# Optimization experiments

Measured on AMD Instinct MI355X. Metric: run time of the kernel, lower is better.

Reference implementation:

```python
import jax, jax.numpy as jnp
import numpy as np

V, E, H, L = 80, 8, 256, 2
B, S = 2048, 256


def setup_inputs() -> dict:
    key = jax.random.key(0)
    ks = jax.random.split(key, 8)
    x = jax.random.randint(ks[0], (B, S), 0, V, dtype=jnp.int32)
    emb = jax.random.normal(ks[1], (V, E), jnp.float32) * 0.1

    def cell_params(k, din):
        k1, k2 = jax.random.split(k)
        W_ih = jax.random.normal(k1, (4 * H, din), jnp.float32) * (1.0 / np.sqrt(din))
        W_hh = jax.random.normal(k2, (4 * H, H), jnp.float32) * (1.0 / np.sqrt(H))
        # biases zero except forget gate (second quarter) set to 1, as in _initialize_weights
        b_ih = jnp.zeros((4 * H,), jnp.float32).at[H:2 * H].set(1.0)
        b_hh = jnp.zeros((4 * H,), jnp.float32).at[H:2 * H].set(1.0)
        return W_ih, W_hh, b_ih, b_hh

    W_ih0, W_hh0, b_ih0, b_hh0 = cell_params(ks[2], E)
    W_ih1, W_hh1, b_ih1, b_hh1 = cell_params(ks[3], H)
    fc_w = jax.random.normal(ks[4], (V, H), jnp.float32) * (1.0 / np.sqrt(H))
    fc_b = jnp.zeros((V,), jnp.float32)
    return dict(x=x, emb=emb,
                W_ih0=W_ih0, W_hh0=W_hh0, b_ih0=b_ih0, b_hh0=b_hh0,
                W_ih1=W_ih1, W_hh1=W_hh1, b_ih1=b_ih1, b_hh1=b_hh1,
                fc_w=fc_w, fc_b=fc_b)


def _lstm_cell(x_t, h, c, W_ih, W_hh, b_ih, b_hh):
    # PyTorch LSTMCell gate order: i, f, g, o
    gates = x_t @ W_ih.T + b_ih + h @ W_hh.T + b_hh  # [B, 4H]
    i_g, f_g, g_g, o_g = jnp.split(gates, 4, axis=-1)
    c_new = jax.nn.sigmoid(f_g) * c + jax.nn.sigmoid(i_g) * jnp.tanh(g_g)
    h_new = jax.nn.sigmoid(o_g) * jnp.tanh(c_new)
    return h_new, c_new


def reference(x, emb, W_ih0, W_hh0, b_ih0, b_hh0, W_ih1, W_hh1, b_ih1, b_hh1, fc_w, fc_b):
    batch = x.shape[0]
    layers = ((W_ih0, W_hh0, b_ih0, b_hh0), (W_ih1, W_hh1, b_ih1, b_hh1))
    e = emb[x]                       # [B, S, E]
    e_t = jnp.swapaxes(e, 0, 1)      # [S, B, E] time-major for scan

    h0 = tuple(jnp.zeros((batch, H), e.dtype) for _ in range(L))
    c0 = tuple(jnp.zeros((batch, H), e.dtype) for _ in range(L))

    def step(carry, x_t):
        hs, cs = carry
        inp = x_t
        new_h, new_c = [], []
        for i, (Wi, Wh, bi, bh) in enumerate(layers):
            h_i, c_i = _lstm_cell(inp, hs[i], cs[i], Wi, Wh, bi, bh)
            new_h.append(h_i)
            new_c.append(c_i)
            inp = h_i
        return (tuple(new_h), tuple(new_c)), None

    (h_fin, c_fin), _ = jax.lax.scan(step, (h0, c0), e_t)
    # dropout is identity in eval mode; fc on last layer's final hidden state
    logits = h_fin[-1] @ fc_w.T + fc_b    # [B, V]
    return logits, (jnp.stack(h_fin), jnp.stack(c_fin))
```

## Files before the change

### kernel.cpp

```cpp
#include <hip/hip_runtime.h>
#include <math.h>

#define VCAB 80
#define EDIM 8
#define HDIM 256
#define BAT 2048
#define SEQ 256
#define BT 8
#define NWG (BAT/BT)
#define NTHR 512

#define W0T_K 264
#define W1T_K 512
#define W0T_OFF 0
#define W1T_OFF (W0T_K*1024)
#define BIAS0_OFF (W1T_OFF + W1T_K*1024)
#define BIAS1_OFF (BIAS0_OFF + 1024)
#define WS_FLOATS (BIAS1_OFF + 1024)

__global__ void prep_kernel(const float* __restrict__ Wih0, const float* __restrict__ Whh0,
                            const float* __restrict__ bih0, const float* __restrict__ bhh0,
                            const float* __restrict__ Wih1, const float* __restrict__ Whh1,
                            const float* __restrict__ bih1, const float* __restrict__ bhh1,
                            float* __restrict__ ws) {
  int idx = blockIdx.x * 256 + threadIdx.x;
  if (idx < W0T_K * 1024) {
    int k = idx >> 10, n2 = idx & 1023;
    int unit = n2 >> 2, g = n2 & 3, r = g * HDIM + unit;
    float v = (k < EDIM) ? Wih0[r * EDIM + k] : Whh0[r * HDIM + (k - EDIM)];
    ws[W0T_OFF + idx] = v;
  } else if (idx < W0T_K * 1024 + W1T_K * 1024) {
    int i2 = idx - W0T_K * 1024;
    int k = i2 >> 10, n2 = i2 & 1023;
    int unit = n2 >> 2, g = n2 & 3, r = g * HDIM + unit;
    float v = (k < HDIM) ? Wih1[r * HDIM + k] : Whh1[r * HDIM + (k - HDIM)];
    ws[W1T_OFF + i2] = v;
  } else if (idx < W0T_K * 1024 + W1T_K * 1024 + 1024) {
    int n2 = idx - (W0T_K * 1024 + W1T_K * 1024);
    int unit = n2 >> 2, g = n2 & 3, r = g * HDIM + unit;
    ws[BIAS0_OFF + n2] = bih0[r] + bhh0[r];
  } else if (idx < W0T_K * 1024 + W1T_K * 1024 + 2048) {
    int n2 = idx - (W0T_K * 1024 + W1T_K * 1024 + 1024);
    int unit = n2 >> 2, g = n2 & 3, r = g * HDIM + unit;
    ws[BIAS1_OFF + n2] = bih1[r] + bhh1[r];
  }
}

__device__ __forceinline__ float sigm(float x) {
  return 1.0f / (1.0f + __expf(-x));
}
__device__ __forceinline__ float tanh_f(float x) {
  float ax = fabsf(x);
  float e = __expf(-2.0f * ax);
  float t = 1.0f - 2.0f * e / (1.0f + e);
  return copysignf(t, x);
}

#define FMA4(A, HS, W) \
  A.x += (HS) * (W).x; A.y += (HS) * (W).y; A.z += (HS) * (W).z; A.w += (HS) * (W).w;

__global__ __launch_bounds__(NTHR, 2) void lstm_kernel(
    const int* __restrict__ x, const float* __restrict__ emb,
    const float* __restrict__ ws,
    const float* __restrict__ fcw, const float* __restrict__ fcb,
    float* __restrict__ out) {
  __shared__ float inp0[BT][W0T_K];
  __shared__ float inp1[BT][W1T_K];
  __shared__ float4 red[BT][HDIM];

  const int tid = threadIdx.x;
  const int grp = tid >> 8;
  const int utid = tid & 255;
  const int bg = blockIdx.x * BT;
  const float4* __restrict__ W0 = (const float4*)(ws + W0T_OFF);
  const float4* __restrict__ W1 = (const float4*)(ws + W1T_OFF);

  float c0[BT], c1[BT];
#pragma unroll
  for (int b = 0; b < BT; b++) { c0[b] = 0.f; c1[b] = 0.f; }
  if (grp == 0) {
#pragma unroll
    for (int b = 0; b < BT; b++) {
      inp0[b][EDIM + utid] = 0.f;
      inp1[b][utid] = 0.f;
      inp1[b][HDIM + utid] = 0.f;
    }
  }
  const float4 bias0 = ((const float4*)(ws + BIAS0_OFF))[utid];
  const float4 bias1 = ((const float4*)(ws + BIAS1_OFF))[utid];
  __syncthreads();

  for (int t = 0; t < SEQ; t++) {
    if (tid < BT * EDIM) {
      int b = tid >> 3, d = tid & 7;
      int xv = x[(bg + b) * SEQ + t];
      inp0[b][d] = emb[xv * EDIM + d];
    }
    __syncthreads();

    float4 acc[BT];
#pragma unroll
    for (int b = 0; b < BT; b++)
      acc[b] = (grp == 0) ? bias0 : make_float4(0.f, 0.f, 0.f, 0.f);
    {
      const int kbase = grp * (W0T_K / 2);
#pragma unroll 3
      for (int i = 0; i < W0T_K / 8; i++) {
        const int k = kbase + 4 * i;
        float4 wa = W0[(k + 0) * 256 + utid];
        float4 wb = W0[(k + 1) * 256 + utid];
        float4 wc = W0[(k + 2) * 256 + utid];
        float4 wd = W0[(k + 3) * 256 + utid];
#pragma unroll
        for (int b = 0; b < BT; b++) {
          float4 hv = *(const float4*)&inp0[b][k];
          FMA4(acc[b], hv.x, wa); FMA4(acc[b], hv.y, wb);
          FMA4(acc[b], hv.z, wc); FMA4(acc[b], hv.w, wd);
        }
      }
    }
    if (grp == 1) {
#pragma unroll
      for (int b = 0; b < BT; b++) red[b][utid] = acc[b];
    }
    __syncthreads();
    if (grp == 0) {
#pragma unroll
      for (int b = 0; b < BT; b++) {
        float4 p = red[b][utid];
        float ig = sigm(acc[b].x + p.x), fg = sigm(acc[b].y + p.y);
        float gg = tanh_f(acc[b].z + p.z), og = sigm(acc[b].w + p.w);
        c0[b] = fg * c0[b] + ig * gg;
        float h = og * tanh_f(c0[b]);
        inp0[b][EDIM + utid] = h;
        inp1[b][utid] = h;
      }
    }
    __syncthreads();

#pragma unroll
    for (int b = 0; b < BT; b++)
      acc[b] = (grp == 0) ? bias1 : make_float4(0.f, 0.f, 0.f, 0.f);
    {
      const int kbase = grp * (W1T_K / 2);
#pragma unroll 4
      for (int i = 0; i < W1T_K / 8; i++) {
        const int k = kbase + 4 * i;
        float4 wa = W1[(k + 0) * 256 + utid];
        float4 wb = W1[(k + 1) * 256 + utid];
        float4 wc = W1[(k + 2) * 256 + utid];
        float4 wd = W1[(k + 3) * 256 + utid];
#pragma unroll
        for (int b = 0; b < BT; b++) {
          float4 hv = *(const float4*)&inp1[b][k];
          FMA4(acc[b], hv.x, wa); FMA4(acc[b], hv.y, wb);
          FMA4(acc[b], hv.z, wc); FMA4(acc[b], hv.w, wd);
        }
      }
    }
    if (grp == 1) {
#pragma unroll
      for (int b = 0; b < BT; b++) red[b][utid] = acc[b];
    }
    __syncthreads();
    if (grp == 0) {
#pragma unroll
      for (int b = 0; b < BT; b++) {
        float4 p = red[b][utid];
        float ig = sigm(acc[b].x + p.x), fg = sigm(acc[b].y + p.y);
        float gg = tanh_f(acc[b].z + p.z), og = sigm(acc[b].w + p.w);
        c1[b] = fg * c1[b] + ig * gg;
        inp1[b][HDIM + utid] = og * tanh_f(c1[b]);
      }
    }
    __syncthreads();
  }

  for (int o = tid; o < BT * VCAB; o += NTHR) {
    int b = o / VCAB, v = o - b * VCAB;
    float a = fcb[v];
    const float4* wrow = (const float4*)(fcw + v * HDIM);
    const float4* hrow = (const float4*)&inp1[b][HDIM];
#pragma unroll 4
    for (int k = 0; k < HDIM / 4; k++) {
      float4 w = wrow[k];
      float4 h = hrow[k];
      a += h.x * w.x + h.y * w.y + h.z * w.z + h.w * w.w;
    }
    out[(bg + b) * VCAB + v] = a;
  }

  if (grp == 0) {
    float* outh = out + BAT * VCAB;
    float* outc = outh + 2 * BAT * HDIM;
#pragma unroll
    for (int b = 0; b < BT; b++) {
      outh[0 * BAT * HDIM + (bg + b) * HDIM + utid] = inp0[b][EDIM + utid];
      outh[1 * BAT * HDIM + (bg + b) * HDIM + utid] = inp1[b][HDIM + utid];
      outc[0 * BAT * HDIM + (bg + b) * HDIM + utid] = c0[b];
      outc[1 * BAT * HDIM + (bg + b) * HDIM + utid] = c1[b];
    }
  }
}

extern "C" void kernel_launch(void* const* d_in, const int* in_sizes, int n_in,
                              void* d_out, int out_size, void* d_ws, size_t ws_size,
                              hipStream_t stream) {
  const int*   x    = (const int*)d_in[0];
  const float* emb  = (const float*)d_in[1];
  const float* Wih0 = (const float*)d_in[2];
  const float* Whh0 = (const float*)d_in[3];
  const float* bih0 = (const float*)d_in[4];
  const float* bhh0 = (const float*)d_in[5];
  const float* Wih1 = (const float*)d_in[6];
  const float* Whh1 = (const float*)d_in[7];
  const float* bih1 = (const float*)d_in[8];
  const float* bhh1 = (const float*)d_in[9];
  const float* fcw  = (const float*)d_in[10];
  const float* fcb  = (const float*)d_in[11];
  float* out = (float*)d_out;
  float* ws  = (float*)d_ws;

  prep_kernel<<<(WS_FLOATS + 255) / 256, 256, 0, stream>>>(
      Wih0, Whh0, bih0, bhh0, Wih1, Whh1, bih1, bhh1, ws);
  lstm_kernel<<<NWG, NTHR, 0, stream>>>(x, emb, ws, fcw, fcb, out);
}
```

Baseline: 14.71 ms.

## Double block size and split batch rows across two thread halves

Block size goes from 512 to 1024 threads. The 8 batch rows of a workgroup are now split into two halves of 4 rows, each handled by its own 512-thread group that keeps the existing two-way K split. Each thread holds fewer accumulators and cell states, which frees registers and exposes more parallelism per step. In exchange, every weight element is loaded twice per block, once per row half, so per-step global/L2 weight traffic doubles and fewer FMAs are amortised per load.

```diff
diff --git a/kernel.cpp b/kernel.cpp
--- a/kernel.cpp
+++ b/kernel.cpp
@@ -8,7 +8,7 @@
 #define SEQ 256
 #define BT 8
 #define NWG (BAT/BT)
-#define NTHR 512
+#define NTHR 1024
 
 #define W0T_K 264
 #define W1T_K 512
@@ -59,7 +59,7 @@
 #define FMA4(A, HS, W) \
   A.x += (HS) * (W).x; A.y += (HS) * (W).y; A.z += (HS) * (W).z; A.w += (HS) * (W).w;
 
-__global__ __launch_bounds__(NTHR, 2) void lstm_kernel(
+__global__ __launch_bounds__(NTHR, 4) void lstm_kernel(
     const int* __restrict__ x, const float* __restrict__ emb,
     const float* __restrict__ ws,
     const float* __restrict__ fcw, const float* __restrict__ fcb,
@@ -69,21 +69,23 @@
   __shared__ float4 red[BT][HDIM];
 
   const int tid = threadIdx.x;
-  const int grp = tid >> 8;
   const int utid = tid & 255;
+  const int kgrp = (tid >> 8) & 1;
+  const int rh = tid >> 9;
+  const int rbase = rh * 4;
   const int bg = blockIdx.x * BT;
   const float4* __restrict__ W0 = (const float4*)(ws + W0T_OFF);
   const float4* __restrict__ W1 = (const float4*)(ws + W1T_OFF);
 
-  float c0[BT], c1[BT];
-#pragma unroll
-  for (int b = 0; b < BT; b++) { c0[b] = 0.f; c1[b] = 0.f; }
-  if (grp == 0) {
-#pragma unroll
-    for (int b = 0; b < BT; b++) {
-      inp0[b][EDIM + utid] = 0.f;
-      inp1[b][utid] = 0.f;
-      inp1[b][HDIM + utid] = 0.f;
+  float c0[4], c1[4];
+#pragma unroll
+  for (int j = 0; j < 4; j++) { c0[j] = 0.f; c1[j] = 0.f; }
+  if (kgrp == 0) {
+#pragma unroll
+    for (int j = 0; j < 4; j++) {
+      inp0[rbase + j][EDIM + utid] = 0.f;
+      inp1[rbase + j][utid] = 0.f;
+      inp1[rbase + j][HDIM + utid] = 0.f;
     }
   }
   const float4 bias0 = ((const float4*)(ws + BIAS0_OFF))[utid];
@@ -98,12 +100,12 @@
     }
     __syncthreads();
 
-    float4 acc[BT];
-#pragma unroll
-    for (int b = 0; b < BT; b++)
-      acc[b] = (grp == 0) ? bias0 : make_float4(0.f, 0.f, 0.f, 0.f);
+    float4 acc[4];
+#pragma unroll
+    for (int j = 0; j < 4; j++)
+      acc[j] = (kgrp == 0) ? bias0 : make_float4(0.f, 0.f, 0.f, 0.f);
     {
-      const int kbase = grp * (W0T_K / 2);
+      const int kbase = kgrp * (W0T_K / 2);
 #pragma unroll 3
       for (int i = 0; i < W0T_K / 8; i++) {
         const int k = kbase + 4 * i;
@@ -112,37 +114,37 @@
         float4 wc = W0[(k + 2) * 256 + utid];
         float4 wd = W0[(k + 3) * 256 + utid];
 #pragma unroll
-        for (int b = 0; b < BT; b++) {
-          float4 hv = *(const float4*)&inp0[b][k];
-          FMA4(acc[b], hv.x, wa); FMA4(acc[b], hv.y, wb);
-          FMA4(acc[b], hv.z, wc); FMA4(acc[b], hv.w, wd);
+        for (int j = 0; j < 4; j++) {
+          float4 hv = *(const float4*)&inp0[rbase + j][k];
+          FMA4(acc[j], hv.x, wa); FMA4(acc[j], hv.y, wb);
+          FMA4(acc[j], hv.z, wc); FMA4(acc[j], hv.w, wd);
         }
       }
     }
-    if (grp == 1) {
-#pragma unroll
-      for (int b = 0; b < BT; b++) red[b][utid] = acc[b];
-    }
-    __syncthreads();
-    if (grp == 0) {
-#pragma unroll
-      for (int b = 0; b < BT; b++) {
-        float4 p = red[b][utid];
-        float ig = sigm(acc[b].x + p.x), fg = sigm(acc[b].y + p.y);
-        float gg = tanh_f(acc[b].z + p.z), og = sigm(acc[b].w + p.w);
-        c0[b] = fg * c0[b] + ig * gg;
-        float h = og * tanh_f(c0[b]);
-        inp0[b][EDIM + utid] = h;
-        inp1[b][utid] = h;
-      }
-    }
-    __syncthreads();
-
-#pragma unroll
-    for (int b = 0; b < BT; b++)
-      acc[b] = (grp == 0) ? bias1 : make_float4(0.f, 0.f, 0.f, 0.f);
+    if (kgrp == 1) {
+#pragma unroll
+      for (int j = 0; j < 4; j++) red[rbase + j][utid] = acc[j];
+    }
+    __syncthreads();
+    if (kgrp == 0) {
+#pragma unroll
+      for (int j = 0; j < 4; j++) {
+        float4 p = red[rbase + j][utid];
+        float ig = sigm(acc[j].x + p.x), fg = sigm(acc[j].y + p.y);
+        float gg = tanh_f(acc[j].z + p.z), og = sigm(acc[j].w + p.w);
+        c0[j] = fg * c0[j] + ig * gg;
+        float h = og * tanh_f(c0[j]);
+        inp0[rbase + j][EDIM + utid] = h;
+        inp1[rbase + j][utid] = h;
+      }
+    }
+    __syncthreads();
+
+#pragma unroll
+    for (int j = 0; j < 4; j++)
+      acc[j] = (kgrp == 0) ? bias1 : make_float4(0.f, 0.f, 0.f, 0.f);
     {
-      const int kbase = grp * (W1T_K / 2);
+      const int kbase = kgrp * (W1T_K / 2);
 #pragma unroll 4
       for (int i = 0; i < W1T_K / 8; i++) {
         const int k = kbase + 4 * i;
@@ -151,26 +153,26 @@
         float4 wc = W1[(k + 2) * 256 + utid];
         float4 wd = W1[(k + 3) * 256 + utid];
 #pragma unroll
-        for (int b = 0; b < BT; b++) {
-          float4 hv = *(const float4*)&inp1[b][k];
-          FMA4(acc[b], hv.x, wa); FMA4(acc[b], hv.y, wb);
-          FMA4(acc[b], hv.z, wc); FMA4(acc[b], hv.w, wd);
+        for (int j = 0; j < 4; j++) {
+          float4 hv = *(const float4*)&inp1[rbase + j][k];
+          FMA4(acc[j], hv.x, wa); FMA4(acc[j], hv.y, wb);
+          FMA4(acc[j], hv.z, wc); FMA4(acc[j], hv.w, wd);
         }
       }
     }
-    if (grp == 1) {
-#pragma unroll
-      for (int b = 0; b < BT; b++) red[b][utid] = acc[b];
-    }
-    __syncthreads();
-    if (grp == 0) {
-#pragma unroll
-      for (int b = 0; b < BT; b++) {
-        float4 p = red[b][utid];
-        float ig = sigm(acc[b].x + p.x), fg = sigm(acc[b].y + p.y);
-        float gg = tanh_f(acc[b].z + p.z), og = sigm(acc[b].w + p.w);
-        c1[b] = fg * c1[b] + ig * gg;
-        inp1[b][HDIM + utid] = og * tanh_f(c1[b]);
+    if (kgrp == 1) {
+#pragma unroll
+      for (int j = 0; j < 4; j++) red[rbase + j][utid] = acc[j];
+    }
+    __syncthreads();
+    if (kgrp == 0) {
+#pragma unroll
+      for (int j = 0; j < 4; j++) {
+        float4 p = red[rbase + j][utid];
+        float ig = sigm(acc[j].x + p.x), fg = sigm(acc[j].y + p.y);
+        float gg = tanh_f(acc[j].z + p.z), og = sigm(acc[j].w + p.w);
+        c1[j] = fg * c1[j] + ig * gg;
+        inp1[rbase + j][HDIM + utid] = og * tanh_f(c1[j]);
       }
     }
     __syncthreads();
@@ -190,15 +192,16 @@
     out[(bg + b) * VCAB + v] = a;
   }
 
-  if (grp == 0) {
+  if (kgrp == 0) {
     float* outh = out + BAT * VCAB;
     float* outc = outh + 2 * BAT * HDIM;
 #pragma unroll
-    for (int b = 0; b < BT; b++) {
+    for (int j = 0; j < 4; j++) {
+      int b = rbase + j;
       outh[0 * BAT * HDIM + (bg + b) * HDIM + utid] = inp0[b][EDIM + utid];
       outh[1 * BAT * HDIM + (bg + b) * HDIM + utid] = inp1[b][HDIM + utid];
-      outc[0 * BAT * HDIM + (bg + b) * HDIM + utid] = c0[b];
-      outc[1 * BAT * HDIM + (bg + b) * HDIM + utid] = c1[b];
+      outc[0 * BAT * HDIM + (bg + b) * HDIM + utid] = c0[j];
+      outc[1 * BAT * HDIM + (bg + b) * HDIM + utid] = c1[j];
     }
   }
 }
```

Result: slower. 16.52 ms (+12.3%).

## Split LSTM K reduction across four thread groups with 1024-thread blocks

Applied to the files above, without the earlier changes.

Raises the workgroup size from 512 to 1024 threads and splits each step's gate matmul K dimension across four groups of 256 threads instead of two. Three groups write partial sums to shared memory and group 0 reduces them and adds the bias. The layer-0 K dimension is padded from 264 to 272 with zero weights so it divides evenly. The aim is more parallelism per recurrent step, at the cost of more shared memory for the reduction buffer, a larger serial reduction in group 0, and tighter register limits from the launch bounds.

```diff
diff --git a/kernel.cpp b/kernel.cpp
--- a/kernel.cpp
+++ b/kernel.cpp
@@ -8,12 +8,13 @@
 #define SEQ 256
 #define BT 8
 #define NWG (BAT/BT)
-#define NTHR 512
-
-#define W0T_K 264
+#define NTHR 1024
+#define KG 4
+
+#define W0T_KP 272
 #define W1T_K 512
 #define W0T_OFF 0
-#define W1T_OFF (W0T_K*1024)
+#define W1T_OFF (W0T_KP*1024)
 #define BIAS0_OFF (W1T_OFF + W1T_K*1024)
 #define BIAS1_OFF (BIAS0_OFF + 1024)
 #define WS_FLOATS (BIAS1_OFF + 1024)
@@ -24,23 +25,25 @@
                             const float* __restrict__ bih1, const float* __restrict__ bhh1,
                             float* __restrict__ ws) {
   int idx = blockIdx.x * 256 + threadIdx.x;
-  if (idx < W0T_K * 1024) {
+  if (idx < W0T_KP * 1024) {
     int k = idx >> 10, n2 = idx & 1023;
     int unit = n2 >> 2, g = n2 & 3, r = g * HDIM + unit;
-    float v = (k < EDIM) ? Wih0[r * EDIM + k] : Whh0[r * HDIM + (k - EDIM)];
+    float v = (k < EDIM) ? Wih0[r * EDIM + k]
+            : (k < EDIM + HDIM) ? Whh0[r * HDIM + (k - EDIM)]
+            : 0.f;
     ws[W0T_OFF + idx] = v;
-  } else if (idx < W0T_K * 1024 + W1T_K * 1024) {
-    int i2 = idx - W0T_K * 1024;
+  } else if (idx < W0T_KP * 1024 + W1T_K * 1024) {
+    int i2 = idx - W0T_KP * 1024;
     int k = i2 >> 10, n2 = i2 & 1023;
     int unit = n2 >> 2, g = n2 & 3, r = g * HDIM + unit;
     float v = (k < HDIM) ? Wih1[r * HDIM + k] : Whh1[r * HDIM + (k - HDIM)];
     ws[W1T_OFF + i2] = v;
-  } else if (idx < W0T_K * 1024 + W1T_K * 1024 + 1024) {
-    int n2 = idx - (W0T_K * 1024 + W1T_K * 1024);
+  } else if (idx < W0T_KP * 1024 + W1T_K * 1024 + 1024) {
+    int n2 = idx - (W0T_KP * 1024 + W1T_K * 1024);
     int unit = n2 >> 2, g = n2 & 3, r = g * HDIM + unit;
     ws[BIAS0_OFF + n2] = bih0[r] + bhh0[r];
-  } else if (idx < W0T_K * 1024 + W1T_K * 1024 + 2048) {
-    int n2 = idx - (W0T_K * 1024 + W1T_K * 1024 + 1024);
+  } else if (idx < W0T_KP * 1024 + W1T_K * 1024 + 2048) {
+    int n2 = idx - (W0T_KP * 1024 + W1T_K * 1024 + 1024);
     int unit = n2 >> 2, g = n2 & 3, r = g * HDIM + unit;
     ws[BIAS1_OFF + n2] = bih1[r] + bhh1[r];
   }
@@ -59,18 +62,18 @@
 #define FMA4(A, HS, W) \
   A.x += (HS) * (W).x; A.y += (HS) * (W).y; A.z += (HS) * (W).z; A.w += (HS) * (W).w;
 
-__global__ __launch_bounds__(NTHR, 2) void lstm_kernel(
+__global__ __launch_bounds__(NTHR, 4) void lstm_kernel(
     const int* __restrict__ x, const float* __restrict__ emb,
     const float* __restrict__ ws,
     const float* __restrict__ fcw, const float* __restrict__ fcb,
     float* __restrict__ out) {
-  __shared__ float inp0[BT][W0T_K];
+  __shared__ float inp0[BT][W0T_KP];
   __shared__ float inp1[BT][W1T_K];
-  __shared__ float4 red[BT][HDIM];
+  __shared__ float4 red[KG - 1][BT][HDIM];
 
   const int tid = threadIdx.x;
-  const int grp = tid >> 8;
   const int utid = tid & 255;
+  const int kgrp = tid >> 8;
   const int bg = blockIdx.x * BT;
   const float4* __restrict__ W0 = (const float4*)(ws + W0T_OFF);
   const float4* __restrict__ W1 = (const float4*)(ws + W1T_OFF);
@@ -78,7 +81,7 @@
   float c0[BT], c1[BT];
 #pragma unroll
   for (int b = 0; b < BT; b++) { c0[b] = 0.f; c1[b] = 0.f; }
-  if (grp == 0) {
+  if (kgrp == 0) {
 #pragma unroll
     for (int b = 0; b < BT; b++) {
       inp0[b][EDIM + utid] = 0.f;
@@ -86,6 +89,7 @@
       inp1[b][HDIM + utid] = 0.f;
     }
   }
+  if (tid < BT * EDIM) inp0[tid >> 3][264 + (tid & 7)] = 0.f;
   const float4 bias0 = ((const float4*)(ws + BIAS0_OFF))[utid];
   const float4 bias1 = ((const float4*)(ws + BIAS1_OFF))[utid];
   __syncthreads();
@@ -100,12 +104,11 @@
 
     float4 acc[BT];
 #pragma unroll
-    for (int b = 0; b < BT; b++)
-      acc[b] = (grp == 0) ? bias0 : make_float4(0.f, 0.f, 0.f, 0.f);
+    for (int b = 0; b < BT; b++) acc[b] = make_float4(0.f, 0.f, 0.f, 0.f);
     {
-      const int kbase = grp * (W0T_K / 2);
-#pragma unroll 3
-      for (int i = 0; i < W0T_K / 8; i++) {
+      const int kbase = kgrp * (W0T_KP / KG);
+#pragma unroll 2
+      for (int i = 0; i < W0T_KP / KG / 4; i++) {
         const int k = kbase + 4 * i;
         float4 wa = W0[(k + 0) * 256 + utid];
         float4 wb = W0[(k + 1) * 256 + utid];
@@ -119,17 +122,20 @@
         }
       }
     }
-    if (grp == 1) {
-#pragma unroll
-      for (int b = 0; b < BT; b++) red[b][utid] = acc[b];
-    }
-    __syncthreads();
-    if (grp == 0) {
+    if (kgrp > 0) {
+#pragma unroll
+      for (int b = 0; b < BT; b++) red[kgrp - 1][b][utid] = acc[b];
+    }
+    __syncthreads();
+    if (kgrp == 0) {
 #pragma unroll
       for (int b = 0; b < BT; b++) {
-        float4 p = red[b][utid];
-        float ig = sigm(acc[b].x + p.x), fg = sigm(acc[b].y + p.y);
-        float gg = tanh_f(acc[b].z + p.z), og = sigm(acc[b].w + p.w);
+        float4 p0 = red[0][b][utid], p1 = red[1][b][utid], p2 = red[2][b][utid];
+        float gx = acc[b].x + p0.x + p1.x + p2.x + bias0.x;
+        float gy = acc[b].y + p0.y + p1.y + p2.y + bias0.y;
+        float gz = acc[b].z + p0.z + p1.z + p2.z + bias0.z;
+        float gw = acc[b].w + p0.w + p1.w + p2.w + bias0.w;
+        float ig = sigm(gx), fg = sigm(gy), gg = tanh_f(gz), og = sigm(gw);
         c0[b] = fg * c0[b] + ig * gg;
         float h = og * tanh_f(c0[b]);
         inp0[b][EDIM + utid] = h;
@@ -139,12 +145,11 @@
     __syncthreads();
 
 #pragma unroll
-    for (int b = 0; b < BT; b++)
-      acc[b] = (grp == 0) ? bias1 : make_float4(0.f, 0.f, 0.f, 0.f);
+    for (int b = 0; b < BT; b++) acc[b] = make_float4(0.f, 0.f, 0.f, 0.f);
     {
-      const int kbase = grp * (W1T_K / 2);
-#pragma unroll 4
-      for (int i = 0; i < W1T_K / 8; i++) {
+      const int kbase = kgrp * (W1T_K / KG);
+#pragma unroll 2
+      for (int i = 0; i < W1T_K / KG / 4; i++) {
         const int k = kbase + 4 * i;
         float4 wa = W1[(k + 0) * 256 + utid];
         float4 wb = W1[(k + 1) * 256 + utid];
@@ -158,17 +163,20 @@
         }
       }
     }
-    if (grp == 1) {
-#pragma unroll
-      for (int b = 0; b < BT; b++) red[b][utid] = acc[b];
-    }
-    __syncthreads();
-    if (grp == 0) {
+    if (kgrp > 0) {
+#pragma unroll
+      for (int b = 0; b < BT; b++) red[kgrp - 1][b][utid] = acc[b];
+    }
+    __syncthreads();
+    if (kgrp == 0) {
 #pragma unroll
       for (int b = 0; b < BT; b++) {
-        float4 p = red[b][utid];
-        float ig = sigm(acc[b].x + p.x), fg = sigm(acc[b].y + p.y);
-        float gg = tanh_f(acc[b].z + p.z), og = sigm(acc[b].w + p.w);
+        float4 p0 = red[0][b][utid], p1 = red[1][b][utid], p2 = red[2][b][utid];
+        float gx = acc[b].x + p0.x + p1.x + p2.x + bias1.x;
+        float gy = acc[b].y + p0.y + p1.y + p2.y + bias1.y;
+        float gz = acc[b].z + p0.z + p1.z + p2.z + bias1.z;
+        float gw = acc[b].w + p0.w + p1.w + p2.w + bias1.w;
+        float ig = sigm(gx), fg = sigm(gy), gg = tanh_f(gz), og = sigm(gw);
         c1[b] = fg * c1[b] + ig * gg;
         inp1[b][HDIM + utid] = og * tanh_f(c1[b]);
       }
@@ -190,7 +198,7 @@
     out[(bg + b) * VCAB + v] = a;
   }
 
-  if (grp == 0) {
+  if (kgrp == 0) {
     float* outh = out + BAT * VCAB;
     float* outc = outh + 2 * BAT * HDIM;
 #pragma unroll
```

Result: faster. 13.70 ms (-6.9%).
